# Performance work log

Measured on AMD Instinct MI355X. Metric: run time of the kernel, lower is better.

Reference implementation:

```python
import jax, jax.numpy as jnp
import numpy as np

N_NODES = 100000
N_EDGES = 1600000
D = 128
L = 3


def setup_inputs() -> dict:
    key = jax.random.key(0)
    k1, k2, k3 = jax.random.split(key, 3)
    edge_index = jax.random.randint(k1, (2, N_EDGES), 0, N_NODES, dtype=jnp.int64)
    emb = jax.random.normal(k2, (N_NODES, D), dtype=jnp.float32)
    # Glorot-style scale for the per-layer linear weights
    Ws = jax.random.normal(k3, (L, D, D), dtype=jnp.float32) * (1.0 / np.sqrt(D))
    bs = jnp.zeros((L, D), dtype=jnp.float32)
    return {"edge_index": edge_index, "emb": emb, "Ws": Ws, "bs": bs}


def _gcn_forward(emb, Ws, bs, edge_index):
    n = emb.shape[0]
    self_loop = jnp.arange(n, dtype=edge_index.dtype)
    # PyG GCNConv adds self-loops and uses symmetric normalization
    row = jnp.concatenate([edge_index[0], self_loop])  # source nodes
    col = jnp.concatenate([edge_index[1], self_loop])  # target nodes
    deg = jax.ops.segment_sum(jnp.ones(row.shape[0], dtype=emb.dtype), col, num_segments=n)
    deg_inv_sqrt = jnp.where(deg > 0, jax.lax.rsqrt(jnp.maximum(deg, 1.0)), 0.0)
    norm = deg_inv_sqrt[row] * deg_inv_sqrt[col]  # [E+N]

    x = emb
    for l in range(Ws.shape[0]):
        h = x @ Ws[l]                              # [N, D] linear transform
        msg = h[row] * norm[:, None]               # gather + scale [E+N, D]
        x = jax.ops.segment_sum(msg, col, num_segments=n) + bs[l]  # scatter-add
        x = jax.nn.relu(x)                         # dropout is identity in eval
    return x


def reference(edge_index, emb, Ws, bs) -> jnp.ndarray:
    return _gcn_forward(emb, Ws, bs, edge_index)
```

## Files before the change

### kernel.cpp

```cpp
#include <hip/hip_runtime.h>
#include <hip/hip_fp16.h>
#include <cstdint>
#include <cstddef>

#define N_NODES 100000
#define N_EDGES 1600000
#define D 128
#define NLAYERS 3
#define NB 3125
#define NBLK_E 128
#define EPB 12500
#define ENT_CAP 1024

typedef float f2v __attribute__((ext_vector_type(2)));
typedef float f4v __attribute__((ext_vector_type(4)));
typedef _Float16 f16x8 __attribute__((ext_vector_type(8)));
typedef float f32x4 __attribute__((ext_vector_type(4)));


__global__ __launch_bounds__(512) void hist1_kernel(const int* __restrict__ col,
                                                    int* __restrict__ hmat) {
    __shared__ int hist[NB];
    int b = blockIdx.x, t = threadIdx.x;
    for (int j = t; j < NB; j += 512) hist[j] = 0;
    __syncthreads();
    int base = b * EPB;
    for (int i = t; i < EPB; i += 512) {
        int c = col[base + i];
        atomicAdd(&hist[c >> 5], 1);
    }
    __syncthreads();
    for (int j = t; j < NB; j += 512) hmat[b * NB + j] = hist[j];
}

__global__ void btot_kernel(const int* __restrict__ hmat, int* __restrict__ btot) {
    int j = blockIdx.x * 256 + threadIdx.x;
    if (j < NB) {
        int s = 0;
        for (int b = 0; b < NBLK_E; b++) s += hmat[b * NB + j];
        btot[j] = s;
    }
}

__global__ void bscan_kernel(const int* __restrict__ btot, int* __restrict__ bstart, int nb, int e) {
    __shared__ int lsum[1024];
    int t = threadIdx.x;
    int vals[4];
    int v0 = 0;
#pragma unroll
    for (int j = 0; j < 4; j++) {
        int idx = t * 4 + j;
        int c = (idx < nb) ? btot[idx] : 0;
        vals[j] = c;
        v0 += c;
    }
    lsum[t] = v0;
    __syncthreads();
    for (int off = 1; off < 1024; off <<= 1) {
        int x = (t >= off) ? lsum[t - off] : 0;
        __syncthreads();
        lsum[t] += x;
        __syncthreads();
    }
    int base = lsum[t] - v0;
#pragma unroll
    for (int j = 0; j < 4; j++) {
        int idx = t * 4 + j;
        if (idx < nb) {
            bstart[idx] = base;
            base += vals[j];
        }
    }
    if (t == 0) bstart[nb] = e;
}

__global__ void hoff_kernel(const int* __restrict__ hmat, const int* __restrict__ bstart,
                            int* __restrict__ hoff) {
    int j = blockIdx.x * 256 + threadIdx.x;
    if (j < NB) {
        int run = bstart[j];
        for (int b = 0; b < NBLK_E; b++) {
            hoff[b * NB + j] = run;
            run += hmat[b * NB + j];
        }
    }
}

__global__ __launch_bounds__(512) void scatter_kernel(const int* __restrict__ row,
                                                      const int* __restrict__ col,
                                                      const int* __restrict__ hoff,
                                                      unsigned* __restrict__ bucketbuf) {
    __shared__ int cur[NB];
    int b = blockIdx.x, t = threadIdx.x;
    for (int j = t; j < NB; j += 512) cur[j] = hoff[b * NB + j];
    __syncthreads();
    int base = b * EPB;
    for (int i = t; i < EPB; i += 512) {
        int r = row[base + i], c = col[base + i];
        int pos = atomicAdd(&cur[c >> 5], 1);
        bucketbuf[pos] = ((unsigned)r << 5) | (unsigned)(c & 31);
    }
}

__global__ void fill2_kernel(const unsigned* __restrict__ bucketbuf, const int* __restrict__ bstart,
                             int* __restrict__ offsets, float* __restrict__ dinv,
                             int* __restrict__ src, int n, int e) {
    __shared__ unsigned ent[ENT_CAP];
    __shared__ int hist[32];
    __shared__ int cur[32];
    __shared__ int loff[32];
    int b = blockIdx.x, t = threadIdx.x;
    int s0 = bstart[b];
    int cnt = bstart[b + 1] - s0;
    if (cnt > ENT_CAP) cnt = ENT_CAP;
    if (t < 32) hist[t] = 0;
    __syncthreads();
    for (int i = t; i < cnt; i += 256) {
        unsigned v = bucketbuf[s0 + i];
        ent[i] = v;
        atomicAdd(&hist[v & 31], 1);
    }
    __syncthreads();
    if (t == 0) {
        int run = s0;
#pragma unroll
        for (int j = 0; j < 32; j++) {
            loff[j] = run;
            run += hist[j];
        }
    }
    __syncthreads();
    if (t < 32) {
        int node = b * 32 + t;
        int o = loff[t];
        offsets[node] = o;
        cur[t] = o;
        dinv[node] = rsqrtf((float)(hist[t] + 1));
    }
    if (b == 0 && t == 0) offsets[n] = e;
    __syncthreads();
    for (int i = t; i < cnt; i += 256) {
        unsigned v = ent[i];
        int pos = atomicAdd(&cur[v & 31], 1);
        src[pos] = (int)(v >> 5);
    }
}


__global__ void cast_kernel(const float2* __restrict__ in, const float* __restrict__ dinv,
                            __half2* __restrict__ out, int n2) {
    int i = blockIdx.x * 256 + threadIdx.x;
    if (i < n2) {
        float d = dinv[i >> 6];
        float2 v = in[i];
        out[i] = __floats2half2_rn(d * v.x, d * v.y);
    }
}

__global__ void wsplit_kernel(const float* __restrict__ W,
                              _Float16* __restrict__ Wh, _Float16* __restrict__ Wl) {
    int c = blockIdx.x, l = blockIdx.y, k = threadIdx.x;
    float w = W[(size_t)l * 16384 + k * 128 + c];
    _Float16 h = (_Float16)w;
    float r = w - (float)h;
    Wh[(size_t)l * 16384 + c * 128 + k] = h;
    Wl[(size_t)l * 16384 + c * 128 + k] = (_Float16)r;
}

__global__ __launch_bounds__(64, 4) void agg_gemm_kernel(
    const __half2* __restrict__ xs_in, const int* __restrict__ offs,
    const int* __restrict__ src, const float* __restrict__ dinv,
    const _Float16* __restrict__ Whp, const _Float16* __restrict__ Wlp,
    const float* __restrict__ bias, float* __restrict__ out,
    __half2* __restrict__ xs_out, int write_h, int write_out) {
    __shared__ _Float16 sA[2][16][136];
    int f = threadIdx.x;
    int r0 = blockIdx.x * 16;

#pragma unroll 1
    for (int lr = 0; lr < 16; lr++) {
        int v = r0 + lr;
        float dv = dinv[v];
        float2 a0 = __half22float2(xs_in[(size_t)v * 64 + f]);
        float ax = a0.x;
        float ay = a0.y;
        int i = offs[v], s1 = offs[v + 1];
        for (; i + 7 < s1; i += 8) {
            int s[8];
#pragma unroll
            for (int j = 0; j < 8; j++) s[j] = src[i + j];
            float2 x[8];
#pragma unroll
            for (int j = 0; j < 8; j++) x[j] = __half22float2(xs_in[(size_t)s[j] * 64 + f]);
#pragma unroll
            for (int j = 0; j < 8; j++) {
                ax += x[j].x;
                ay += x[j].y;
            }
        }
        if (i < s1) {
            int last = s1 - 1;
            int s[8];
            float m[8];
#pragma unroll
            for (int j = 0; j < 8; j++) {
                int idx = i + j;
                bool in = idx < s1;
                s[j] = src[in ? idx : last];
                m[j] = in ? 1.0f : 0.0f;
            }
            float2 x[8];
#pragma unroll
            for (int j = 0; j < 8; j++) x[j] = __half22float2(xs_in[(size_t)s[j] * 64 + f]);
#pragma unroll
            for (int j = 0; j < 8; j++) {
                ax += m[j] * x[j].x;
                ay += m[j] * x[j].y;
            }
        }
        float rx = dv * ax, ry = dv * ay;
        __half2 h2 = __floats2half2_rn(rx, ry);
        float2 hb = __half22float2(h2);
        __half2 l2 = __floats2half2_rn(rx - hb.x, ry - hb.y);
        *(unsigned*)&sA[0][lr][2 * f] = __builtin_bit_cast(unsigned, h2);
        *(unsigned*)&sA[1][lr][2 * f] = __builtin_bit_cast(unsigned, l2);
    }
    __syncthreads();

    int lrow = f & 15, kg = f >> 4;
    f32x4 acc[8];
#pragma unroll
    for (int nf = 0; nf < 8; nf++) acc[nf] = (f32x4){0.f, 0.f, 0.f, 0.f};

#pragma unroll
    for (int ks = 0; ks < 4; ks++) {
        int g = ks * 4 + kg;
        f16x8 ah = *(const f16x8*)&sA[0][lrow][g * 8];
        f16x8 al = *(const f16x8*)&sA[1][lrow][g * 8];
#pragma unroll
        for (int nf = 0; nf < 8; nf++) {
            int col = nf * 16 + lrow;
            f16x8 bh = *(const f16x8*)&Whp[(size_t)col * 128 + g * 8];
            acc[nf] = __builtin_amdgcn_mfma_f32_16x16x32_f16(ah, bh, acc[nf], 0, 0, 0);
            acc[nf] = __builtin_amdgcn_mfma_f32_16x16x32_f16(al, bh, acc[nf], 0, 0, 0);
        }
#pragma unroll
        for (int nf = 0; nf < 8; nf++) {
            int col = nf * 16 + lrow;
            f16x8 bl = *(const f16x8*)&Wlp[(size_t)col * 128 + g * 8];
            acc[nf] = __builtin_amdgcn_mfma_f32_16x16x32_f16(ah, bl, acc[nf], 0, 0, 0);
        }
    }

    float bcol[8];
#pragma unroll
    for (int nf = 0; nf < 8; nf++) bcol[nf] = bias[nf * 16 + lrow];
    int rbase = r0 + kg * 4;
#pragma unroll
    for (int j = 0; j < 4; j++) {
        int rowi = rbase + j;
        float dvr = write_h ? dinv[rowi] : 0.f;
#pragma unroll
        for (int nf = 0; nf < 8; nf++) {
            float o = fmaxf(acc[nf][j] + bcol[nf], 0.f);
            float o2 = __shfl_xor(o, 1);
            int col = nf * 16 + lrow;
            if (write_out)
                __builtin_nontemporal_store(o, out + (size_t)rowi * 128 + col);
            if (write_h && !(f & 1))
                xs_out[(size_t)rowi * 64 + (col >> 1)] =
                    __floats2half2_rn(dvr * o, dvr * o2);
        }
    }
}


extern "C" void kernel_launch(void* const* d_in, const int* in_sizes, int n_in,
                              void* d_out, int out_size, void* d_ws, size_t ws_size,
                              hipStream_t stream) {
    const int* edge = (const int*)d_in[0];
    const float* emb = (const float*)d_in[1];
    const float* Ws = (const float*)d_in[2];
    const float* bs = (const float*)d_in[3];
    float* out = (float*)d_out;

    const int n = N_NODES, e = N_EDGES;
    const int* row = edge;
    const int* col = edge + e;

    char* p = (char*)d_ws;
    __half2* xsA = (__half2*)p;
    unsigned* bucketbuf = (unsigned*)p;
    p += (size_t)n * D * 2;
    __half2* xsB = (__half2*)p;
    p += (size_t)n * D * 2;
    int* csr_src  = (int*)p;    p += (size_t)e * 4;
    float* dinv   = (float*)p;  p += (size_t)n * 4;
    int* offsets  = (int*)p;    p += (size_t)(n + 1) * 4;
    int* btot     = (int*)p;    p += (size_t)NB * 4;
    int* bstart   = (int*)p;    p += (size_t)(NB + 1) * 4;
    int* hmat     = (int*)p;    p += (size_t)NBLK_E * NB * 4;
    int* hoff     = (int*)p;    p += (size_t)NBLK_E * NB * 4;
    _Float16* WhT = (_Float16*)p; p += (size_t)NLAYERS * D * D * 2;
    _Float16* WlT = (_Float16*)p; p += (size_t)NLAYERS * D * D * 2;

    hist1_kernel<<<NBLK_E, 512, 0, stream>>>(col, hmat);
    btot_kernel<<<(NB + 255) / 256, 256, 0, stream>>>(hmat, btot);
    bscan_kernel<<<1, 1024, 0, stream>>>(btot, bstart, NB, e);
    hoff_kernel<<<(NB + 255) / 256, 256, 0, stream>>>(hmat, bstart, hoff);
    scatter_kernel<<<NBLK_E, 512, 0, stream>>>(row, col, hoff, bucketbuf);
    fill2_kernel<<<NB, 256, 0, stream>>>(bucketbuf, bstart, offsets, dinv, csr_src, n, e);
    wsplit_kernel<<<dim3(128, NLAYERS), 128, 0, stream>>>(Ws, WhT, WlT);

    int n2 = n * 64;
    cast_kernel<<<(n2 + 255) / 256, 256, 0, stream>>>((const float2*)emb, dinv, xsA, n2);

    __half2* xin = xsA;
    __half2* xout = xsB;
    for (int l = 0; l < NLAYERS; l++) {
        agg_gemm_kernel<<<n / 16, 64, 0, stream>>>(
            xin, offsets, csr_src, dinv,
            WhT + (size_t)l * D * D, WlT + (size_t)l * D * D,
            bs + (size_t)l * D, out, xout,
            (l < NLAYERS - 1) ? 1 : 0, (l == NLAYERS - 1) ? 1 : 0);
        __half2* tmp = xin; xin = xout; xout = tmp;
    }
}
```

Baseline: 544.7 us.

## Split agg-gemm block across four waves for rows and output columns

Moves the fused aggregate+GEMM kernel from one wave per block to four waves. Each wave aggregates 4 of the 16 rows, then computes 2 of the 8 output column tiles with MFMA. The goal is to cut the serial per-block latency of gathering 16 rows and to spread MFMA work across waves, giving more latency hiding per CU. The cost is larger blocks that share LDS, plus a sync that now waits on four waves.

```diff
diff --git a/kernel.cpp b/kernel.cpp
--- a/kernel.cpp
+++ b/kernel.cpp
@@ -167,18 +167,21 @@
     Wl[(size_t)l * 16384 + c * 128 + k] = (_Float16)r;
 }
 
-__global__ __launch_bounds__(64, 4) void agg_gemm_kernel(
+__global__ __launch_bounds__(256, 8) void agg_gemm_kernel(
     const __half2* __restrict__ xs_in, const int* __restrict__ offs,
     const int* __restrict__ src, const float* __restrict__ dinv,
     const _Float16* __restrict__ Whp, const _Float16* __restrict__ Wlp,
     const float* __restrict__ bias, float* __restrict__ out,
     __half2* __restrict__ xs_out, int write_h, int write_out) {
     __shared__ _Float16 sA[2][16][136];
-    int f = threadIdx.x;
+    int t = threadIdx.x;
+    int f = t & 63;
+    int w = t >> 6;
     int r0 = blockIdx.x * 16;
 
 #pragma unroll 1
-    for (int lr = 0; lr < 16; lr++) {
+    for (int q = 0; q < 4; q++) {
+        int lr = w * 4 + q;
         int v = r0 + lr;
         float dv = dinv[v];
         float2 a0 = __half22float2(xs_in[(size_t)v * 64 + f]);
@@ -228,9 +231,9 @@
     __syncthreads();
 
     int lrow = f & 15, kg = f >> 4;
-    f32x4 acc[8];
-#pragma unroll
-    for (int nf = 0; nf < 8; nf++) acc[nf] = (f32x4){0.f, 0.f, 0.f, 0.f};
+    f32x4 acc[2];
+    acc[0] = (f32x4){0.f, 0.f, 0.f, 0.f};
+    acc[1] = (f32x4){0.f, 0.f, 0.f, 0.f};
 
 #pragma unroll
     for (int ks = 0; ks < 4; ks++) {
@@ -238,33 +241,29 @@
         f16x8 ah = *(const f16x8*)&sA[0][lrow][g * 8];
         f16x8 al = *(const f16x8*)&sA[1][lrow][g * 8];
 #pragma unroll
-        for (int nf = 0; nf < 8; nf++) {
-            int col = nf * 16 + lrow;
+        for (int c = 0; c < 2; c++) {
+            int col = (w * 2 + c) * 16 + lrow;
             f16x8 bh = *(const f16x8*)&Whp[(size_t)col * 128 + g * 8];
-            acc[nf] = __builtin_amdgcn_mfma_f32_16x16x32_f16(ah, bh, acc[nf], 0, 0, 0);
-            acc[nf] = __builtin_amdgcn_mfma_f32_16x16x32_f16(al, bh, acc[nf], 0, 0, 0);
-        }
-#pragma unroll
-        for (int nf = 0; nf < 8; nf++) {
-            int col = nf * 16 + lrow;
             f16x8 bl = *(const f16x8*)&Wlp[(size_t)col * 128 + g * 8];
-            acc[nf] = __builtin_amdgcn_mfma_f32_16x16x32_f16(ah, bl, acc[nf], 0, 0, 0);
-        }
-    }
-
-    float bcol[8];
-#pragma unroll
-    for (int nf = 0; nf < 8; nf++) bcol[nf] = bias[nf * 16 + lrow];
+            acc[c] = __builtin_amdgcn_mfma_f32_16x16x32_f16(ah, bh, acc[c], 0, 0, 0);
+            acc[c] = __builtin_amdgcn_mfma_f32_16x16x32_f16(al, bh, acc[c], 0, 0, 0);
+            acc[c] = __builtin_amdgcn_mfma_f32_16x16x32_f16(ah, bl, acc[c], 0, 0, 0);
+        }
+    }
+
+    float bcol[2];
+    bcol[0] = bias[(w * 2 + 0) * 16 + lrow];
+    bcol[1] = bias[(w * 2 + 1) * 16 + lrow];
     int rbase = r0 + kg * 4;
 #pragma unroll
     for (int j = 0; j < 4; j++) {
         int rowi = rbase + j;
         float dvr = write_h ? dinv[rowi] : 0.f;
 #pragma unroll
-        for (int nf = 0; nf < 8; nf++) {
-            float o = fmaxf(acc[nf][j] + bcol[nf], 0.f);
+        for (int c = 0; c < 2; c++) {
+            float o = fmaxf(acc[c][j] + bcol[c], 0.f);
             float o2 = __shfl_xor(o, 1);
-            int col = nf * 16 + lrow;
+            int col = (w * 2 + c) * 16 + lrow;
             if (write_out)
                 __builtin_nontemporal_store(o, out + (size_t)rowi * 128 + col);
             if (write_h && !(f & 1))
@@ -318,7 +317,7 @@
     __half2* xin = xsA;
     __half2* xout = xsB;
     for (int l = 0; l < NLAYERS; l++) {
-        agg_gemm_kernel<<<n / 16, 64, 0, stream>>>(
+        agg_gemm_kernel<<<n / 16, 256, 0, stream>>>(
             xin, offsets, csr_src, dinv,
             WhT + (size_t)l * D * D, WlT + (size_t)l * D * D,
             bs + (size_t)l * D, out, xout,
```

New measurement: 496.3 us. -8.9%, faster.
